# Performance work log

Measured on AMD Instinct MI355X. Metric: run time of the kernel, lower is better.

## Reference

```python
import jax, jax.numpy as jnp
import numpy as np

IM = 416            # Config.im_w == Config.im_h
IOU_THRESH = 0.6    # Config.iou_thresh
ALPHA_COORD = 5.0   # Config.alpha_coord
ALPHA_NOOBJ = 0.5   # Config.alpha_noobj


def setup_inputs() -> dict:
    key = jax.random.key(0)
    k1, k2, k3, k4, k5, k6 = jax.random.split(key, 6)
    B, S, A, C = 128, 26, 5, 20
    pred_vec = jax.random.normal(k1, (B, S, S, A, 5 + C), dtype=jnp.float32)
    M = 30
    x1 = jax.random.uniform(k2, (B, M)) * 200.0
    y1 = jax.random.uniform(k3, (B, M)) * 200.0
    w = jax.random.uniform(k4, (B, M)) * 190.0 + 10.0
    h = jax.random.uniform(k5, (B, M)) * 190.0 + 10.0
    flag = (jax.random.uniform(k6, (B, M)) < 0.7).astype(jnp.float32)
    target_vec = jnp.stack([x1, y1, w, h, flag], axis=-1)
    anchors = jnp.array([[1.3221, 1.73145], [3.19275, 4.00944], [5.05587, 8.09892],
                         [9.47112, 4.84053], [11.2364, 10.0071]], dtype=jnp.float32)
    return {"pred_vec": pred_vec, "target_vec": target_vec, "anchors": anchors}


def reference(pred_vec, target_vec, anchors):
    Bt, S, _, A, D = pred_vec.shape
    cw = IM // S
    ch = IM // S
    P = S * S * A
    dt = pred_vec.dtype
    sig = jax.nn.sigmoid

    # decode predictions (note: source applies sigmoid*0.5 to w/h channels)
    pred_loc = jnp.concatenate([sig(pred_vec[..., :2]), sig(pred_vec[..., 2:4]) * 0.5], axis=-1)
    pred_conf = sig(pred_vec[..., 4:5])

    gy, gx = jnp.meshgrid(jnp.arange(S, dtype=dt), jnp.arange(S, dtype=dt), indexing='ij')
    pl = jax.lax.stop_gradient(pred_loc)          # .detach() in source
    anc = jax.lax.stop_gradient(anchors)
    bx = (pl[..., 0] + gx[None, :, :, None]) * cw  # [Bt,S,S,A]
    by = (pl[..., 1] + gy[None, :, :, None]) * ch
    bw = jnp.exp(pl[..., 2]) * anc[:, 0] * cw
    bh = jnp.exp(pl[..., 3]) * anc[:, 1] * ch
    pbox = jnp.stack([bx, by, bw, bh], axis=-1).reshape(Bt, P, 4)  # center format

    t = jax.lax.stop_gradient(target_vec)          # targets built without grad in source
    gxc = t[..., 0] + t[..., 2] / 2
    gyc = t[..., 1] + t[..., 3] / 2
    gw = t[..., 2] - t[..., 0]                     # faithful to source (its gt width formula)
    gh = t[..., 3] * t[..., 1]                     # faithful to source (its gt height formula)
    valid = t[..., 4] == 1                          # [Bt,M]

    # IoU between GT [Bt,M] and pred boxes [Bt,P], center format, as bbox_ious()
    g_x1 = gxc - gw / 2; g_x2 = gxc + gw / 2
    g_y1 = gyc - gh / 2; g_y2 = gyc + gh / 2
    p_x1 = pbox[..., 0] - pbox[..., 2] / 2; p_x2 = pbox[..., 0] + pbox[..., 2] / 2
    p_y1 = pbox[..., 1] - pbox[..., 3] / 2; p_y2 = pbox[..., 1] + pbox[..., 3] / 2
    dx = jnp.clip(jnp.minimum(g_x2[:, :, None], p_x2[:, None, :]) -
                  jnp.maximum(g_x1[:, :, None], p_x1[:, None, :]), 0.0)
    dy = jnp.clip(jnp.minimum(g_y2[:, :, None], p_y2[:, None, :]) -
                  jnp.maximum(g_y1[:, :, None], p_y1[:, None, :]), 0.0)
    inter = dx * dy                                 # [Bt,M,P]
    area_g = gw * gh
    area_p = pbox[..., 2] * pbox[..., 3]
    union = area_g[:, :, None] + area_p[:, None, :] - inter
    iou = inter / (union + 1e-9)

    iou_v = jnp.where(valid[:, :, None], iou, 0.0)
    obj = (iou_v > IOU_THRESH).any(axis=1)          # [Bt,P]
    conf_mask = obj.astype(dt)[..., None]           # [Bt,P,1]
    target_conf = conf_mask
    noobj_mask = 1.0 - conf_mask

    # per-annotation responsible cell/anchor via argmax over flattened [S,S,A]
    idx = jnp.argmax(iou, axis=2)                   # [Bt,M]
    ra = idx % A
    rw = (idx // A) % S
    rh = idx // (A * S)
    tx = (gxc - rw.astype(dt) * cw) / cw
    ty = (gyc - rh.astype(dt) * ch) / ch
    tw = jnp.log((t[..., 2] / cw) / anc[ra, 0])
    th = jnp.log((t[..., 3] / ch) / anc[ra, 1])
    vals = jnp.stack([tx, ty, tw, th], axis=-1)     # [Bt,M,4]

    flat = jnp.where(valid, idx, P)                 # route invalid annos out of bounds
    bidx = jnp.arange(Bt)[:, None]
    target_loc = jnp.zeros((Bt, P, 4), dt).at[bidx, flat].set(vals, mode='drop')
    loc_mask = jnp.zeros((Bt, P, 4), dt).at[bidx, flat].set(1.0, mode='drop')

    pl_f = pred_loc.reshape(Bt, P, 4)
    pc_f = pred_conf.reshape(Bt, P, 1)
    loss_loc = ALPHA_COORD * jnp.sum((pl_f * loc_mask - target_loc * loc_mask) ** 2) / Bt
    loss_conf = (jnp.sum((pc_f * conf_mask - target_conf * conf_mask) ** 2) +
                 ALPHA_NOOBJ * jnp.sum((pc_f * noobj_mask) ** 2)) / Bt
    loss_tot = loss_loc + loss_conf
    return jnp.stack([loss_tot, loss_loc, loss_conf])
```

## Files before the change

kernel.cpp:

```cpp
#include <hip/hip_runtime.h>
#include <math.h>

namespace {

constexpr int kS = 26;
constexpr int kA = 5;
constexpr int kP = kS * kS * kA;
constexpr int kM = 30;
constexpr int kB = 128;
constexpr float kCW = 16.0f;
constexpr int kThreads = 512;
constexpr int kWaves = kThreads / 64;
constexpr int kMaskW = (kP + 31) / 32;

__device__ __forceinline__ float sig(float x) { return 1.0f / (1.0f + expf(-x)); }

__global__ __launch_bounds__(kThreads) void loss_main(
    const float* __restrict__ pred,
    const float* __restrict__ targ,
    const float* __restrict__ anch,
    float* __restrict__ ws) {
  __shared__ float4 sbox[kP];
  __shared__ unsigned int sobj[kMaskW];
  __shared__ float t_raw[kM * 5];
  __shared__ float g_x1[kM], g_x2[kM], g_y1[kM], g_y2[kM], g_area[kM];
  __shared__ int s_valid[kM];
  __shared__ int s_idx[kM];
  __shared__ float s_anc[2 * kA];
  __shared__ float red[kWaves][3];

  const int b = blockIdx.x;
  const int tid = threadIdx.x;
  const int lane = tid & 63;
  const int wid = tid >> 6;

  if (tid < 2 * kA) s_anc[tid] = anch[tid];
  if (tid < kM * 5) t_raw[tid] = targ[b * (kM * 5) + tid];
  for (int i = tid; i < kMaskW; i += kThreads) sobj[i] = 0u;
  __syncthreads();

  if (tid < kM) {
    const float t0 = t_raw[tid * 5 + 0];
    const float t1 = t_raw[tid * 5 + 1];
    const float t2 = t_raw[tid * 5 + 2];
    const float t3 = t_raw[tid * 5 + 3];
    const float t4 = t_raw[tid * 5 + 4];
    const float gxc = t0 + t2 * 0.5f;
    const float gyc = t1 + t3 * 0.5f;
    const float gw = t2 - t0;
    const float gh = t3 * t1;
    g_x1[tid] = gxc - gw * 0.5f;
    g_x2[tid] = gxc + gw * 0.5f;
    g_y1[tid] = gyc - gh * 0.5f;
    g_y2[tid] = gyc + gh * 0.5f;
    g_area[tid] = gw * gh;
    s_valid[tid] = (t4 == 1.0f) ? 1 : 0;
  }
  __syncthreads();

  float c2_all = 0.0f;
  for (int p = tid; p < kP; p += kThreads) {
    const float* pp = pred + (b * kP + p) * 25;
    const float s0 = sig(pp[0]);
    const float s1 = sig(pp[1]);
    const float s2 = sig(pp[2]) * 0.5f;
    const float s3 = sig(pp[3]) * 0.5f;
    const float c = sig(pp[4]);
    c2_all += c * c;
    const int a = p % kA;
    const int gx = (p / kA) % kS;
    const int gy = p / (kA * kS);
    float4 box;
    box.x = (s0 + (float)gx) * kCW;
    box.y = (s1 + (float)gy) * kCW;
    box.z = expf(s2) * s_anc[2 * a + 0] * kCW;
    box.w = expf(s3) * s_anc[2 * a + 1] * kCW;
    sbox[p] = box;
  }
  __syncthreads();

  for (int m = wid; m < kM; m += kWaves) {
    if (!s_valid[m]) continue;
    const float gx1 = g_x1[m], gx2 = g_x2[m];
    const float gy1 = g_y1[m], gy2 = g_y2[m];
    const float ga = g_area[m];
    float best = -INFINITY;
    int bi = 0;
    for (int p = lane; p < kP; p += 64) {
      const float4 box = sbox[p];
      const float hw = box.z * 0.5f, hh = box.w * 0.5f;
      const float px1 = box.x - hw, px2 = box.x + hw;
      const float py1 = box.y - hh, py2 = box.y + hh;
      float dx = fminf(gx2, px2) - fmaxf(gx1, px1);
      float dy = fminf(gy2, py2) - fmaxf(gy1, py1);
      dx = fmaxf(dx, 0.0f);
      dy = fmaxf(dy, 0.0f);
      const float inter = dx * dy;
      const float uni = ga + box.z * box.w - inter;
      const float iou = inter / (uni + 1e-9f);
      if (iou > 0.6f) atomicOr(&sobj[p >> 5], 1u << (p & 31));
      if (iou > best) { best = iou; bi = p; }
    }
#pragma unroll
    for (int off = 32; off > 0; off >>= 1) {
      const float ob = __shfl_down(best, off);
      const int oi = __shfl_down(bi, off);
      if (ob > best || (ob == best && oi < bi)) { best = ob; bi = oi; }
    }
    if (lane == 0) s_idx[m] = bi;
  }
  __syncthreads();

  float obj_term = 0.0f, obj_c2 = 0.0f;
  for (int w = tid; w < kMaskW; w += kThreads) {
    unsigned int bits = sobj[w];
    while (bits) {
      const int bit = __ffs(bits) - 1;
      bits &= bits - 1;
      const int p = (w << 5) | bit;
      const float c = sig(pred[(b * kP + p) * 25 + 4]);
      const float d = c - 1.0f;
      obj_term += d * d;
      obj_c2 += c * c;
    }
  }

  float loc = 0.0f;
  if (tid < kM && s_valid[tid]) {
    const int m = tid;
    const int idx = s_idx[m];
    bool live = true;
    for (int m2 = m + 1; m2 < kM; ++m2) {
      if (s_valid[m2] && s_idx[m2] == idx) { live = false; break; }
    }
    if (live) {
      const float t0 = t_raw[m * 5 + 0];
      const float t1 = t_raw[m * 5 + 1];
      const float t2 = t_raw[m * 5 + 2];
      const float t3 = t_raw[m * 5 + 3];
      const float gxc = t0 + t2 * 0.5f;
      const float gyc = t1 + t3 * 0.5f;
      const int ra = idx % kA;
      const int rw = (idx / kA) % kS;
      const int rh = idx / (kA * kS);
      const float tx = (gxc - (float)rw * kCW) / kCW;
      const float ty = (gyc - (float)rh * kCW) / kCW;
      const float tw = logf((t2 / kCW) / s_anc[2 * ra + 0]);
      const float th = logf((t3 / kCW) / s_anc[2 * ra + 1]);
      const float* pp = pred + (b * kP + idx) * 25;
      const float d0 = sig(pp[0]) - tx;
      const float d1 = sig(pp[1]) - ty;
      const float d2 = sig(pp[2]) * 0.5f - tw;
      const float d3 = sig(pp[3]) * 0.5f - th;
      loc = d0 * d0 + d1 * d1 + d2 * d2 + d3 * d3;
    }
  }

  float v0 = obj_term;
  float v1 = c2_all - obj_c2;
  float v2 = loc;
#pragma unroll
  for (int off = 32; off > 0; off >>= 1) {
    v0 += __shfl_down(v0, off);
    v1 += __shfl_down(v1, off);
    v2 += __shfl_down(v2, off);
  }
  if (lane == 0) { red[wid][0] = v0; red[wid][1] = v1; red[wid][2] = v2; }
  __syncthreads();
  if (tid == 0) {
    float a0 = 0.f, a1 = 0.f, a2 = 0.f;
    for (int w = 0; w < kWaves; ++w) { a0 += red[w][0]; a1 += red[w][1]; a2 += red[w][2]; }
    ws[b * 3 + 0] = a0;
    ws[b * 3 + 1] = a1;
    ws[b * 3 + 2] = a2;
  }
}

__global__ __launch_bounds__(kB) void loss_final(const float* __restrict__ ws,
                                                 float* __restrict__ out) {
  __shared__ float red[2][3];
  const int tid = threadIdx.x;
  float a0 = ws[tid * 3 + 0];
  float a1 = ws[tid * 3 + 1];
  float a2 = ws[tid * 3 + 2];
#pragma unroll
  for (int off = 32; off > 0; off >>= 1) {
    a0 += __shfl_down(a0, off);
    a1 += __shfl_down(a1, off);
    a2 += __shfl_down(a2, off);
  }
  if ((tid & 63) == 0) {
    red[tid >> 6][0] = a0;
    red[tid >> 6][1] = a1;
    red[tid >> 6][2] = a2;
  }
  __syncthreads();
  if (tid == 0) {
    const float obj = red[0][0] + red[1][0];
    const float noobj = red[0][1] + red[1][1];
    const float locs = red[0][2] + red[1][2];
    const float loss_conf = (obj + 0.5f * noobj) / (float)kB;
    const float loss_loc = 5.0f * locs / (float)kB;
    out[0] = loss_loc + loss_conf;
    out[1] = loss_loc;
    out[2] = loss_conf;
  }
}

}

extern "C" void kernel_launch(void* const* d_in, const int* in_sizes, int n_in,
                              void* d_out, int out_size, void* d_ws, size_t ws_size,
                              hipStream_t stream) {
  const float* pred = (const float*)d_in[0];
  const float* targ = (const float*)d_in[1];
  const float* anch = (const float*)d_in[2];
  float* out = (float*)d_out;
  float* ws = (float*)d_ws;
  loss_main<<<kB, kThreads, 0, stream>>>(pred, targ, anch, ws);
  loss_final<<<1, kB, 0, stream>>>(ws, out);
}
```

Before: 121.1 us.

## Split per-image loss across many blocks with atomic packed-key argmax

```diff
diff --git a/kernel.cpp b/kernel.cpp
--- a/kernel.cpp
+++ b/kernel.cpp
@@ -9,198 +9,182 @@
 constexpr int kM = 30;
 constexpr int kB = 128;
 constexpr float kCW = 16.0f;
-constexpr int kThreads = 512;
-constexpr int kWaves = kThreads / 64;
-constexpr int kMaskW = (kP + 31) / 32;
+constexpr int kTA = 256;
+constexpr int kChunks = (kP + kTA - 1) / kTA;
+
+constexpr size_t kKeyBytes = (size_t)kB * kM * 8;
+constexpr size_t kZeroBytes = kKeyBytes + 3 * sizeof(float);
 
 __device__ __forceinline__ float sig(float x) { return 1.0f / (1.0f + expf(-x)); }
 
-__global__ __launch_bounds__(kThreads) void loss_main(
-    const float* __restrict__ pred,
-    const float* __restrict__ targ,
-    const float* __restrict__ anch,
-    float* __restrict__ ws) {
-  __shared__ float4 sbox[kP];
-  __shared__ unsigned int sobj[kMaskW];
-  __shared__ float t_raw[kM * 5];
-  __shared__ float g_x1[kM], g_x2[kM], g_y1[kM], g_y2[kM], g_area[kM];
+__device__ __forceinline__ unsigned long long pack_key(float f, int p) {
+  unsigned int u = __float_as_uint(f);
+  unsigned int k = (f >= 0.0f) ? (u | 0x80000000u) : ~u;
+  return ((unsigned long long)k << 32) |
+         (unsigned long long)(0xFFFFFFFFu - (unsigned)p);
+}
+
+__global__ __launch_bounds__(kTA) void loss_A(
+    const float* __restrict__ pred, const float* __restrict__ targ,
+    const float* __restrict__ anch, unsigned long long* __restrict__ keys,
+    float* __restrict__ accum) {
+  __shared__ float s_gx1[kM], s_gx2[kM], s_gy1[kM], s_gy2[kM], s_ga[kM];
   __shared__ int s_valid[kM];
-  __shared__ int s_idx[kM];
   __shared__ float s_anc[2 * kA];
-  __shared__ float red[kWaves][3];
-
-  const int b = blockIdx.x;
+  __shared__ float s_red[kTA / 64][2];
+
+  const int b = blockIdx.y;
   const int tid = threadIdx.x;
+  const int p = blockIdx.x * kTA + tid;
   const int lane = tid & 63;
   const int wid = tid >> 6;
 
   if (tid < 2 * kA) s_anc[tid] = anch[tid];
-  if (tid < kM * 5) t_raw[tid] = targ[b * (kM * 5) + tid];
-  for (int i = tid; i < kMaskW; i += kThreads) sobj[i] = 0u;
-  __syncthreads();
-
   if (tid < kM) {
-    const float t0 = t_raw[tid * 5 + 0];
-    const float t1 = t_raw[tid * 5 + 1];
-    const float t2 = t_raw[tid * 5 + 2];
-    const float t3 = t_raw[tid * 5 + 3];
-    const float t4 = t_raw[tid * 5 + 4];
+    const float t0 = targ[b * kM * 5 + tid * 5 + 0];
+    const float t1 = targ[b * kM * 5 + tid * 5 + 1];
+    const float t2 = targ[b * kM * 5 + tid * 5 + 2];
+    const float t3 = targ[b * kM * 5 + tid * 5 + 3];
+    const float t4 = targ[b * kM * 5 + tid * 5 + 4];
     const float gxc = t0 + t2 * 0.5f;
     const float gyc = t1 + t3 * 0.5f;
     const float gw = t2 - t0;
     const float gh = t3 * t1;
-    g_x1[tid] = gxc - gw * 0.5f;
-    g_x2[tid] = gxc + gw * 0.5f;
-    g_y1[tid] = gyc - gh * 0.5f;
-    g_y2[tid] = gyc + gh * 0.5f;
-    g_area[tid] = gw * gh;
+    s_gx1[tid] = gxc - gw * 0.5f;
+    s_gx2[tid] = gxc + gw * 0.5f;
+    s_gy1[tid] = gyc - gh * 0.5f;
+    s_gy2[tid] = gyc + gh * 0.5f;
+    s_ga[tid] = gw * gh;
     s_valid[tid] = (t4 == 1.0f) ? 1 : 0;
   }
   __syncthreads();
 
-  float c2_all = 0.0f;
-  for (int p = tid; p < kP; p += kThreads) {
-    const float* pp = pred + (b * kP + p) * 25;
+  const bool active = (p < kP);
+  float4 box = make_float4(0.f, 0.f, 0.f, 0.f);
+  float c = 0.0f;
+  if (active) {
+    const float* pp = pred + ((size_t)b * kP + p) * 25;
     const float s0 = sig(pp[0]);
     const float s1 = sig(pp[1]);
     const float s2 = sig(pp[2]) * 0.5f;
     const float s3 = sig(pp[3]) * 0.5f;
-    const float c = sig(pp[4]);
-    c2_all += c * c;
+    c = sig(pp[4]);
     const int a = p % kA;
     const int gx = (p / kA) % kS;
     const int gy = p / (kA * kS);
-    float4 box;
     box.x = (s0 + (float)gx) * kCW;
     box.y = (s1 + (float)gy) * kCW;
     box.z = expf(s2) * s_anc[2 * a + 0] * kCW;
     box.w = expf(s3) * s_anc[2 * a + 1] * kCW;
-    sbox[p] = box;
-  }
-  __syncthreads();
-
-  for (int m = wid; m < kM; m += kWaves) {
+  }
+  const float hw = box.z * 0.5f, hh = box.w * 0.5f;
+  const float px1 = box.x - hw, px2 = box.x + hw;
+  const float py1 = box.y - hh, py2 = box.y + hh;
+  const float ap = box.z * box.w;
+
+  bool obj = false;
+  for (int m = 0; m < kM; ++m) {
     if (!s_valid[m]) continue;
-    const float gx1 = g_x1[m], gx2 = g_x2[m];
-    const float gy1 = g_y1[m], gy2 = g_y2[m];
-    const float ga = g_area[m];
-    float best = -INFINITY;
-    int bi = 0;
-    for (int p = lane; p < kP; p += 64) {
-      const float4 box = sbox[p];
-      const float hw = box.z * 0.5f, hh = box.w * 0.5f;
-      const float px1 = box.x - hw, px2 = box.x + hw;
-      const float py1 = box.y - hh, py2 = box.y + hh;
-      float dx = fminf(gx2, px2) - fmaxf(gx1, px1);
-      float dy = fminf(gy2, py2) - fmaxf(gy1, py1);
-      dx = fmaxf(dx, 0.0f);
-      dy = fmaxf(dy, 0.0f);
-      const float inter = dx * dy;
-      const float uni = ga + box.z * box.w - inter;
-      const float iou = inter / (uni + 1e-9f);
-      if (iou > 0.6f) atomicOr(&sobj[p >> 5], 1u << (p & 31));
-      if (iou > best) { best = iou; bi = p; }
+    float dx = fminf(s_gx2[m], px2) - fmaxf(s_gx1[m], px1);
+    float dy = fminf(s_gy2[m], py2) - fmaxf(s_gy1[m], py1);
+    dx = fmaxf(dx, 0.0f);
+    dy = fmaxf(dy, 0.0f);
+    const float inter = dx * dy;
+    const float iou = inter / (s_ga[m] + ap - inter + 1e-9f);
+    const bool pos = active && (iou > 0.0f);
+    obj = obj || (iou > 0.6f && active);
+    if (__any(pos)) {
+      unsigned long long k = pos ? pack_key(iou, p) : 0ull;
+#pragma unroll
+      for (int off = 32; off > 0; off >>= 1) {
+        const unsigned long long o = __shfl_down(k, off);
+        if (o > k) k = o;
+      }
+      if (lane == 0) atomicMax(&keys[b * kM + m], k);
     }
-#pragma unroll
-    for (int off = 32; off > 0; off >>= 1) {
-      const float ob = __shfl_down(best, off);
-      const int oi = __shfl_down(bi, off);
-      if (ob > best || (ob == best && oi < bi)) { best = ob; bi = oi; }
+  }
+
+  float objt = 0.0f, noob = 0.0f;
+  if (active) {
+    if (obj) {
+      const float d = c - 1.0f;
+      objt = d * d;
+    } else {
+      noob = c * c;
     }
-    if (lane == 0) s_idx[m] = bi;
-  }
-  __syncthreads();
-
-  float obj_term = 0.0f, obj_c2 = 0.0f;
-  for (int w = tid; w < kMaskW; w += kThreads) {
-    unsigned int bits = sobj[w];
-    while (bits) {
-      const int bit = __ffs(bits) - 1;
-      bits &= bits - 1;
-      const int p = (w << 5) | bit;
-      const float c = sig(pred[(b * kP + p) * 25 + 4]);
-      const float d = c - 1.0f;
-      obj_term += d * d;
-      obj_c2 += c * c;
-    }
-  }
-
-  float loc = 0.0f;
-  if (tid < kM && s_valid[tid]) {
-    const int m = tid;
-    const int idx = s_idx[m];
-    bool live = true;
-    for (int m2 = m + 1; m2 < kM; ++m2) {
-      if (s_valid[m2] && s_idx[m2] == idx) { live = false; break; }
-    }
-    if (live) {
-      const float t0 = t_raw[m * 5 + 0];
-      const float t1 = t_raw[m * 5 + 1];
-      const float t2 = t_raw[m * 5 + 2];
-      const float t3 = t_raw[m * 5 + 3];
-      const float gxc = t0 + t2 * 0.5f;
-      const float gyc = t1 + t3 * 0.5f;
-      const int ra = idx % kA;
-      const int rw = (idx / kA) % kS;
-      const int rh = idx / (kA * kS);
-      const float tx = (gxc - (float)rw * kCW) / kCW;
-      const float ty = (gyc - (float)rh * kCW) / kCW;
-      const float tw = logf((t2 / kCW) / s_anc[2 * ra + 0]);
-      const float th = logf((t3 / kCW) / s_anc[2 * ra + 1]);
-      const float* pp = pred + (b * kP + idx) * 25;
-      const float d0 = sig(pp[0]) - tx;
-      const float d1 = sig(pp[1]) - ty;
-      const float d2 = sig(pp[2]) * 0.5f - tw;
-      const float d3 = sig(pp[3]) * 0.5f - th;
-      loc = d0 * d0 + d1 * d1 + d2 * d2 + d3 * d3;
-    }
-  }
-
-  float v0 = obj_term;
-  float v1 = c2_all - obj_c2;
-  float v2 = loc;
+  }
 #pragma unroll
   for (int off = 32; off > 0; off >>= 1) {
-    v0 += __shfl_down(v0, off);
-    v1 += __shfl_down(v1, off);
-    v2 += __shfl_down(v2, off);
-  }
-  if (lane == 0) { red[wid][0] = v0; red[wid][1] = v1; red[wid][2] = v2; }
+    objt += __shfl_down(objt, off);
+    noob += __shfl_down(noob, off);
+  }
+  if (lane == 0) {
+    s_red[wid][0] = objt;
+    s_red[wid][1] = noob;
+  }
   __syncthreads();
   if (tid == 0) {
-    float a0 = 0.f, a1 = 0.f, a2 = 0.f;
-    for (int w = 0; w < kWaves; ++w) { a0 += red[w][0]; a1 += red[w][1]; a2 += red[w][2]; }
-    ws[b * 3 + 0] = a0;
-    ws[b * 3 + 1] = a1;
-    ws[b * 3 + 2] = a2;
-  }
-}
-
-__global__ __launch_bounds__(kB) void loss_final(const float* __restrict__ ws,
-                                                 float* __restrict__ out) {
-  __shared__ float red[2][3];
-  const int tid = threadIdx.x;
-  float a0 = ws[tid * 3 + 0];
-  float a1 = ws[tid * 3 + 1];
-  float a2 = ws[tid * 3 + 2];
+    float a0 = 0.f, a1 = 0.f;
+    for (int w = 0; w < kTA / 64; ++w) {
+      a0 += s_red[w][0];
+      a1 += s_red[w][1];
+    }
+    atomicAdd(&accum[0], a0);
+    atomicAdd(&accum[1], a1);
+  }
+}
+
+__global__ __launch_bounds__(64) void loss_B(
+    const float* __restrict__ pred, const float* __restrict__ targ,
+    const float* __restrict__ anch, const unsigned long long* __restrict__ keys,
+    float* __restrict__ accum) {
+  const int b = blockIdx.x;
+  const int m = threadIdx.x;
+  int idx = -1;
+  int valid = 0;
+  float t0 = 0.f, t1 = 0.f, t2 = 0.f, t3 = 0.f;
+  if (m < kM) {
+    const unsigned long long k = keys[b * kM + m];
+    idx = (k == 0ull) ? 0 : (int)(0xFFFFFFFFu - (unsigned)(k & 0xFFFFFFFFull));
+    t0 = targ[b * kM * 5 + m * 5 + 0];
+    t1 = targ[b * kM * 5 + m * 5 + 1];
+    t2 = targ[b * kM * 5 + m * 5 + 2];
+    t3 = targ[b * kM * 5 + m * 5 + 3];
+    valid = (targ[b * kM * 5 + m * 5 + 4] == 1.0f) ? 1 : 0;
+  }
+  bool dead = false;
+  for (int j = 1; j < kM; ++j) {
+    const int idx2 = __shfl(idx, j);
+    const int v2 = __shfl(valid, j);
+    if (j > m && v2 && idx2 == idx) dead = true;
+  }
+  float loc = 0.0f;
+  if (m < kM && valid && !dead) {
+    const float gxc = t0 + t2 * 0.5f;
+    const float gyc = t1 + t3 * 0.5f;
+    const int ra = idx % kA;
+    const int rw = (idx / kA) % kS;
+    const int rh = idx / (kA * kS);
+    const float tx = (gxc - (float)rw * kCW) / kCW;
+    const float ty = (gyc - (float)rh * kCW) / kCW;
+    const float tw = logf((t2 / kCW) / anch[2 * ra + 0]);
+    const float th = logf((t3 / kCW) / anch[2 * ra + 1]);
+    const float* pp = pred + ((size_t)b * kP + idx) * 25;
+    const float d0 = sig(pp[0]) - tx;
+    const float d1 = sig(pp[1]) - ty;
+    const float d2 = sig(pp[2]) * 0.5f - tw;
+    const float d3 = sig(pp[3]) * 0.5f - th;
+    loc = d0 * d0 + d1 * d1 + d2 * d2 + d3 * d3;
+  }
 #pragma unroll
-  for (int off = 32; off > 0; off >>= 1) {
-    a0 += __shfl_down(a0, off);
-    a1 += __shfl_down(a1, off);
-    a2 += __shfl_down(a2, off);
-  }
-  if ((tid & 63) == 0) {
-    red[tid >> 6][0] = a0;
-    red[tid >> 6][1] = a1;
-    red[tid >> 6][2] = a2;
-  }
-  __syncthreads();
-  if (tid == 0) {
-    const float obj = red[0][0] + red[1][0];
-    const float noobj = red[0][1] + red[1][1];
-    const float locs = red[0][2] + red[1][2];
-    const float loss_conf = (obj + 0.5f * noobj) / (float)kB;
-    const float loss_loc = 5.0f * locs / (float)kB;
+  for (int off = 32; off > 0; off >>= 1) loc += __shfl_down(loc, off);
+  if (m == 0) atomicAdd(&accum[2], loc);
+}
+
+__global__ void loss_C(const float* __restrict__ accum, float* __restrict__ out) {
+  if (threadIdx.x == 0) {
+    const float loss_conf = (accum[0] + 0.5f * accum[1]) / (float)kB;
+    const float loss_loc = 5.0f * accum[2] / (float)kB;
     out[0] = loss_loc + loss_conf;
     out[1] = loss_loc;
     out[2] = loss_conf;
@@ -216,7 +200,11 @@
   const float* targ = (const float*)d_in[1];
   const float* anch = (const float*)d_in[2];
   float* out = (float*)d_out;
-  float* ws = (float*)d_ws;
-  loss_main<<<kB, kThreads, 0, stream>>>(pred, targ, anch, ws);
-  loss_final<<<1, kB, 0, stream>>>(ws, out);
-}
+  unsigned long long* keys = (unsigned long long*)d_ws;
+  float* accum = (float*)((char*)d_ws + kKeyBytes);
+
+  hipMemsetAsync(d_ws, 0, kZeroBytes, stream);
+  loss_A<<<dim3(kChunks, kB), kTA, 0, stream>>>(pred, targ, anch, keys, accum);
+  loss_B<<<kB, 64, 0, stream>>>(pred, targ, anch, keys, accum);
+  loss_C<<<1, 64, 0, stream>>>(accum, out);
+}
```

Result: slower. 139.3 us (+15.0%).
